# Optimization experiments

Measured on AMD Instinct MI355X. Metric: run time of the kernel, lower is better.

The kernel has to match this reference:

```python
import jax, jax.numpy as jnp
import numpy as np

_EPS = 1e-6


def setup_inputs() -> dict:
    key = jax.random.key(0)
    k1, k2, k3, k4 = jax.random.split(key, 4)
    B, N = 32, 131072
    xyz_s = jax.random.normal(k1, (B, 3, N), dtype=jnp.float32)
    weighted_t = jax.random.normal(k2, (B, 3, N), dtype=jnp.float32)
    weights = jax.random.uniform(k3, (B, 1, N), dtype=jnp.float32)
    label = jax.random.randint(k4, (B, 1, N), 0, 2).astype(jnp.float32)
    return {"xyz_s": xyz_s, "weighted_t": weighted_t, "weights": weights, "label": label}


def reference(xyz_s, weighted_t, weights, label):
    # background mask: |label - 1|
    background = jnp.abs(label - 1.0)            # (B,1,N)
    w = (weights * background)[:, 0, :]          # (B,N)
    xs = jnp.swapaxes(xyz_s, 1, 2)               # (B,N,3) source points
    xt = jnp.swapaxes(weighted_t, 1, 2)          # (B,N,3) target points

    # normalized weights
    wn = w[..., None] / (jnp.sum(w, axis=1, keepdims=True)[..., None] + _EPS)  # (B,N,1)

    # weighted centroids
    centroid_s = jnp.sum(xs * wn, axis=1)        # (B,3)
    centroid_t = jnp.sum(xt * wn, axis=1)        # (B,3)

    s_centered = xs - centroid_s[:, None, :]
    t_centered = xt - centroid_t[:, None, :]

    # weighted covariance: s_centered^T @ (t_centered * wn) -> (B,3,3)
    cov = jnp.einsum('bnd,bne->bde', s_centered, t_centered * wn)

    u, s, vh = jnp.linalg.svd(cov)               # cov = u @ diag(s) @ vh
    v = jnp.swapaxes(vh, -1, -2)
    ut = jnp.swapaxes(u, -1, -2)

    rot_pos = v @ ut
    v_neg = v.at[:, :, 2].multiply(-1.0)         # flip last column of V
    rot_neg = v_neg @ ut
    det_pos = jnp.linalg.det(rot_pos)
    rot = jnp.where(det_pos[:, None, None] > 0, rot_pos, rot_neg)  # (B,3,3)

    translation = -rot @ centroid_s[..., None] + centroid_t[..., None]  # (B,3,1)
    return rot, translation
```

## Files before the change

kernel.cpp:

```cpp
#include <hip/hip_runtime.h>
#include <math.h>

#define N_PTS 131072
#define BPB   64
#define CHUNK (N_PTS / BPB)
#define TPB   256
#define NACC  16
#define NITER (CHUNK / 4 / TPB)

__global__ __launch_bounds__(TPB) void ego_partial_kernel(
    const float* __restrict__ xyz_s,
    const float* __restrict__ wtgt,
    const float* __restrict__ weights,
    const float* __restrict__ label,
    float* __restrict__ partials)
{
    const int b     = blockIdx.y;
    const int chunk = blockIdx.x;
    const int t     = threadIdx.x;

    const size_t baseN  = (size_t)b * N_PTS + (size_t)chunk * CHUNK;
    const size_t base3  = (size_t)b * 3 * N_PTS + (size_t)chunk * CHUNK;

    const float4* w4  = (const float4*)(weights + baseN);
    const float4* l4  = (const float4*)(label   + baseN);
    const float4* xs0 = (const float4*)(xyz_s + base3);
    const float4* xs1 = (const float4*)(xyz_s + base3 + N_PTS);
    const float4* xs2 = (const float4*)(xyz_s + base3 + 2 * N_PTS);
    const float4* xt0 = (const float4*)(wtgt  + base3);
    const float4* xt1 = (const float4*)(wtgt  + base3 + N_PTS);
    const float4* xt2 = (const float4*)(wtgt  + base3 + 2 * N_PTS);

    float acc[NACC];
#pragma unroll
    for (int i = 0; i < NACC; ++i) acc[i] = 0.0f;

#pragma unroll
    for (int k = 0; k < NITER; ++k) {
        const int i = t + k * TPB;
        const float4 wv = w4[i];
        const float4 lv = l4[i];
        const float4 a0 = xs0[i], a1 = xs1[i], a2 = xs2[i];
        const float4 b0 = xt0[i], b1 = xt1[i], b2 = xt2[i];

#define ACCUM(C)                                              \
        {                                                     \
            const float w  = wv.C * fabsf(lv.C - 1.0f);       \
            const float s0 = a0.C, s1 = a1.C, s2 = a2.C;      \
            const float t0 = b0.C, t1 = b1.C, t2 = b2.C;      \
            acc[0] += w;                                      \
            const float ws0 = w * s0, ws1 = w * s1, ws2 = w * s2; \
            acc[1] += ws0;  acc[2] += ws1;  acc[3] += ws2;    \
            acc[4] += w * t0; acc[5] += w * t1; acc[6] += w * t2; \
            acc[7]  += ws0 * t0; acc[8]  += ws0 * t1; acc[9]  += ws0 * t2; \
            acc[10] += ws1 * t0; acc[11] += ws1 * t1; acc[12] += ws1 * t2; \
            acc[13] += ws2 * t0; acc[14] += ws2 * t1; acc[15] += ws2 * t2; \
        }
        ACCUM(x) ACCUM(y) ACCUM(z) ACCUM(w)
#undef ACCUM
    }

#pragma unroll
    for (int i = 0; i < NACC; ++i) {
        float v = acc[i];
#pragma unroll
        for (int off = 32; off > 0; off >>= 1)
            v += __shfl_down(v, off, 64);
        acc[i] = v;
    }

    __shared__ float red[TPB / 64][NACC];
    const int wave = t >> 6;
    const int lane = t & 63;
    if (lane == 0) {
#pragma unroll
        for (int i = 0; i < NACC; ++i) red[wave][i] = acc[i];
    }
    __syncthreads();

    if (t < NACC) {
        float v = 0.0f;
#pragma unroll
        for (int wv_ = 0; wv_ < TPB / 64; ++wv_) v += red[wv_][t];
        partials[((size_t)b * BPB + chunk) * NACC + t] = v;
    }
}

__global__ __launch_bounds__(64) void ego_finalize_kernel(
    const float* __restrict__ partials,
    float* __restrict__ out,
    int B)
{
    const int b = blockIdx.x;
    const int t = threadIdx.x;

    double acc[NACC];
    const float* p = partials + ((size_t)b * BPB + t) * NACC;
#pragma unroll
    for (int i = 0; i < NACC; ++i) acc[i] = (double)p[i];

#pragma unroll
    for (int i = 0; i < NACC; ++i) {
        double v = acc[i];
#pragma unroll
        for (int off = 32; off > 0; off >>= 1)
            v += __shfl_down(v, off, 64);
        acc[i] = v;
    }

    if (t != 0) return;

    const double W     = acc[0];
    const double denom = W + 1e-6;
    const double cs0 = acc[1] / denom, cs1 = acc[2] / denom, cs2 = acc[3] / denom;
    const double ct0 = acc[4] / denom, ct1 = acc[5] / denom, ct2 = acc[6] / denom;
    const double f   = 2.0 - W / denom;

    const double c00 = acc[7]  / denom - cs0 * ct0 * f;
    const double c01 = acc[8]  / denom - cs0 * ct1 * f;
    const double c02 = acc[9]  / denom - cs0 * ct2 * f;
    const double c10 = acc[10] / denom - cs1 * ct0 * f;
    const double c11 = acc[11] / denom - cs1 * ct1 * f;
    const double c12 = acc[12] / denom - cs1 * ct2 * f;
    const double c20 = acc[13] / denom - cs2 * ct0 * f;
    const double c21 = acc[14] / denom - cs2 * ct1 * f;
    const double c22 = acc[15] / denom - cs2 * ct2 * f;

    double b00 = c00*c00 + c10*c10 + c20*c20;
    double b01 = c00*c01 + c10*c11 + c20*c21;
    double b02 = c00*c02 + c10*c12 + c20*c22;
    double b11 = c01*c01 + c11*c11 + c21*c21;
    double b12 = c01*c02 + c11*c12 + c21*c22;
    double b22 = c02*c02 + c12*c12 + c22*c22;

    double v00 = 1, v01 = 0, v02 = 0;
    double v10 = 0, v11 = 1, v12 = 0;
    double v20 = 0, v21 = 0, v22 = 1;

#define JROT(bpp, bqq, bpq, bkp, bkq, vp0, vp1, vp2, vq0, vq1, vq2)   \
    if (fabs(bpq) > 1e-30) {                                          \
        const double tau = (bqq - bpp) / (2.0 * bpq);                 \
        const double jt  = (tau >= 0.0 ? 1.0 : -1.0) /                \
                           (fabs(tau) + sqrt(1.0 + tau * tau));       \
        const double jc  = 1.0 / sqrt(1.0 + jt * jt);                 \
        const double js  = jt * jc;                                   \
        bpp -= jt * bpq; bqq += jt * bpq; bpq = 0.0;                  \
        { const double kp = bkp, kq = bkq;                            \
          bkp = jc * kp - js * kq; bkq = js * kp + jc * kq; }         \
        { double x;                                                   \
          x = vp0; vp0 = jc * x - js * vq0; vq0 = js * x + jc * vq0;  \
          x = vp1; vp1 = jc * x - js * vq1; vq1 = js * x + jc * vq1;  \
          x = vp2; vp2 = jc * x - js * vq2; vq2 = js * x + jc * vq2; }\
    }

#pragma unroll
    for (int sweep = 0; sweep < 6; ++sweep) {
        JROT(b00, b11, b01, b02, b12, v00, v10, v20, v01, v11, v21)
        JROT(b00, b22, b02, b01, b12, v00, v10, v20, v02, v12, v22)
        JROT(b11, b22, b12, b01, b02, v01, v11, v21, v02, v12, v22)
    }
#undef JROT

    double l0 = b00, l1 = b11, l2 = b22;
#define CSWAP(la, lb, a0, a1, a2, q0, q1, q2)                         \
    if (lb > la) { double x;                                          \
        x = la; la = lb; lb = x;                                      \
        x = a0; a0 = q0; q0 = x;                                      \
        x = a1; a1 = q1; q1 = x;                                      \
        x = a2; a2 = q2; q2 = x; }
    CSWAP(l0, l1, v00, v10, v20, v01, v11, v21)
    CSWAP(l0, l2, v00, v10, v20, v02, v12, v22)
    CSWAP(l1, l2, v01, v11, v21, v02, v12, v22)
#undef CSWAP

#define MAKEU(vc0, vc1, vc2, u0, u1, u2)                              \
    double u0 = c00 * vc0 + c01 * vc1 + c02 * vc2;                    \
    double u1 = c10 * vc0 + c11 * vc1 + c12 * vc2;                    \
    double u2 = c20 * vc0 + c21 * vc1 + c22 * vc2;                    \
    { const double nn = sqrt(u0 * u0 + u1 * u1 + u2 * u2);            \
      const double r = (nn > 1e-150) ? 1.0 / nn : 0.0;                \
      u0 *= r; u1 *= r; u2 *= r; }
    MAKEU(v00, v10, v20, u00, u10, u20)
    MAKEU(v01, v11, v21, u01, u11, u21)
    MAKEU(v02, v12, v22, u02, u12, u22)
#undef MAKEU
    if (u02 * u02 + u12 * u12 + u22 * u22 < 0.5) {
        u02 = u10 * u21 - u20 * u11;
        u12 = u20 * u01 - u00 * u21;
        u22 = u00 * u11 - u10 * u01;
    }

    const double a00_ = v00*u00 + v01*u01, g00 = v02*u02;
    const double a01_ = v00*u10 + v01*u11, g01 = v02*u12;
    const double a02_ = v00*u20 + v01*u21, g02 = v02*u22;
    const double a10_ = v10*u00 + v11*u01, g10 = v12*u02;
    const double a11_ = v10*u10 + v11*u11, g11 = v12*u12;
    const double a12_ = v10*u20 + v11*u21, g12 = v12*u22;
    const double a20_ = v20*u00 + v21*u01, g20 = v22*u02;
    const double a21_ = v20*u10 + v21*u11, g21 = v22*u12;
    const double a22_ = v20*u20 + v21*u21, g22 = v22*u22;

    const double r00 = a00_ + g00, r01 = a01_ + g01, r02 = a02_ + g02;
    const double r10 = a10_ + g10, r11 = a11_ + g11, r12 = a12_ + g12;
    const double r20 = a20_ + g20, r21 = a21_ + g21, r22 = a22_ + g22;
    const double det = r00 * (r11 * r22 - r12 * r21)
                     - r01 * (r10 * r22 - r12 * r20)
                     + r02 * (r10 * r21 - r11 * r20);
    const double sgn = (det > 0.0) ? 1.0 : -1.0;

    const double R00 = a00_ + sgn * g00, R01 = a01_ + sgn * g01, R02 = a02_ + sgn * g02;
    const double R10 = a10_ + sgn * g10, R11 = a11_ + sgn * g11, R12 = a12_ + sgn * g12;
    const double R20 = a20_ + sgn * g20, R21 = a21_ + sgn * g21, R22 = a22_ + sgn * g22;

    const double t0 = -(R00 * cs0 + R01 * cs1 + R02 * cs2) + ct0;
    const double t1 = -(R10 * cs0 + R11 * cs1 + R12 * cs2) + ct1;
    const double t2 = -(R20 * cs0 + R21 * cs1 + R22 * cs2) + ct2;

    float* ro = out + (size_t)b * 9;
    ro[0] = (float)R00; ro[1] = (float)R01; ro[2] = (float)R02;
    ro[3] = (float)R10; ro[4] = (float)R11; ro[5] = (float)R12;
    ro[6] = (float)R20; ro[7] = (float)R21; ro[8] = (float)R22;
    float* to = out + (size_t)B * 9 + (size_t)b * 3;
    to[0] = (float)t0; to[1] = (float)t1; to[2] = (float)t2;
}

extern "C" void kernel_launch(void* const* d_in, const int* in_sizes, int n_in,
                              void* d_out, int out_size, void* d_ws, size_t ws_size,
                              hipStream_t stream) {
    const float* xyz_s   = (const float*)d_in[0];
    const float* wtgt    = (const float*)d_in[1];
    const float* weights = (const float*)d_in[2];
    const float* label   = (const float*)d_in[3];
    float* out = (float*)d_out;
    float* partials = (float*)d_ws;

    const int B = in_sizes[2] / N_PTS;

    dim3 grid1(BPB, B);
    ego_partial_kernel<<<grid1, TPB, 0, stream>>>(xyz_s, wtgt, weights, label, partials);
    ego_finalize_kernel<<<B, 64, 0, stream>>>(partials, out, B);
}
```

Before: 155.3 us.

## Stage chunk inputs into LDS via async global_load_lds before accumulation

Each wave now loads two of the eight input streams directly into shared memory with the global_load_lds builtin, and all threads then read the float4 data from LDS for the moment accumulation. The intent is to issue all global loads up front without spending VGPRs, and to get more memory requests in flight. This adds 64KB of LDS per block, which limits occupancy, plus an extra LDS round trip and a barrier. The reduction scratch now reuses the same LDS buffer. CHUNK is hardcoded to 2048, which still equals N_PTS/BPB.

```diff
diff --git a/kernel.cpp b/kernel.cpp
--- a/kernel.cpp
+++ b/kernel.cpp
@@ -3,10 +3,12 @@
 
 #define N_PTS 131072
 #define BPB   64
-#define CHUNK (N_PTS / BPB)
+#define CHUNK 2048
 #define TPB   256
 #define NACC  16
-#define NITER (CHUNK / 4 / TPB)
+
+typedef const __attribute__((address_space(1))) void gvoid_t;
+typedef __attribute__((address_space(3))) void lvoid_t;
 
 __global__ __launch_bounds__(TPB) void ego_partial_kernel(
     const float* __restrict__ xyz_s,
@@ -15,33 +17,62 @@
     const float* __restrict__ label,
     float* __restrict__ partials)
 {
-    const int b     = blockIdx.y;
-    const int chunk = blockIdx.x;
-    const int t     = threadIdx.x;
-
-    const size_t baseN  = (size_t)b * N_PTS + (size_t)chunk * CHUNK;
-    const size_t base3  = (size_t)b * 3 * N_PTS + (size_t)chunk * CHUNK;
-
-    const float4* w4  = (const float4*)(weights + baseN);
-    const float4* l4  = (const float4*)(label   + baseN);
-    const float4* xs0 = (const float4*)(xyz_s + base3);
-    const float4* xs1 = (const float4*)(xyz_s + base3 + N_PTS);
-    const float4* xs2 = (const float4*)(xyz_s + base3 + 2 * N_PTS);
-    const float4* xt0 = (const float4*)(wtgt  + base3);
-    const float4* xt1 = (const float4*)(wtgt  + base3 + N_PTS);
-    const float4* xt2 = (const float4*)(wtgt  + base3 + 2 * N_PTS);
+    __shared__ __align__(16) float lds[8][CHUNK];
+
+    const int b    = blockIdx.y;
+    const int c    = blockIdx.x;
+    const int t    = threadIdx.x;
+    const int wave = t >> 6;
+    const int lane = t & 63;
+
+    const size_t baseN = (size_t)b * N_PTS + (size_t)c * CHUNK;
+    const size_t base3 = (size_t)b * 3 * N_PTS + (size_t)c * CHUNK;
+
+    const float* g0;
+    const float* g1;
+    switch (wave) {
+        case 0:  g0 = weights + baseN;           g1 = label + baseN;            break;
+        case 1:  g0 = xyz_s + base3;             g1 = xyz_s + base3 + N_PTS;    break;
+        case 2:  g0 = xyz_s + base3 + 2*N_PTS;   g1 = wtgt  + base3;            break;
+        default: g0 = wtgt  + base3 + N_PTS;     g1 = wtgt  + base3 + 2*N_PTS;  break;
+    }
+    float* l0 = &lds[2 * wave][0];
+    float* l1 = &lds[2 * wave + 1][0];
+
+#pragma unroll
+    for (int j = 0; j < 8; ++j) {
+        const int off = j * 256 + lane * 4;
+        __builtin_amdgcn_global_load_lds((gvoid_t*)(g0 + off),
+                                         (lvoid_t*)(l0 + j * 256), 16, 0, 0);
+    }
+#pragma unroll
+    for (int j = 0; j < 8; ++j) {
+        const int off = j * 256 + lane * 4;
+        __builtin_amdgcn_global_load_lds((gvoid_t*)(g1 + off),
+                                         (lvoid_t*)(l1 + j * 256), 16, 0, 0);
+    }
+    __syncthreads();
+
+    const float4* W4 = (const float4*)lds[0];
+    const float4* L4 = (const float4*)lds[1];
+    const float4* A0 = (const float4*)lds[2];
+    const float4* A1 = (const float4*)lds[3];
+    const float4* A2 = (const float4*)lds[4];
+    const float4* B0 = (const float4*)lds[5];
+    const float4* B1 = (const float4*)lds[6];
+    const float4* B2 = (const float4*)lds[7];
 
     float acc[NACC];
 #pragma unroll
     for (int i = 0; i < NACC; ++i) acc[i] = 0.0f;
 
 #pragma unroll
-    for (int k = 0; k < NITER; ++k) {
+    for (int k = 0; k < CHUNK / 4 / TPB; ++k) {
         const int i = t + k * TPB;
-        const float4 wv = w4[i];
-        const float4 lv = l4[i];
-        const float4 a0 = xs0[i], a1 = xs1[i], a2 = xs2[i];
-        const float4 b0 = xt0[i], b1 = xt1[i], b2 = xt2[i];
+        const float4 wv = W4[i];
+        const float4 lv = L4[i];
+        const float4 a0 = A0[i], a1 = A1[i], a2 = A2[i];
+        const float4 b0 = B0[i], b1 = B1[i], b2 = B2[i];
 
 #define ACCUM(C)                                              \
         {                                                     \
@@ -69,20 +100,19 @@
         acc[i] = v;
     }
 
-    __shared__ float red[TPB / 64][NACC];
-    const int wave = t >> 6;
-    const int lane = t & 63;
+    __syncthreads();
+    float* red = (float*)lds;
     if (lane == 0) {
 #pragma unroll
-        for (int i = 0; i < NACC; ++i) red[wave][i] = acc[i];
+        for (int i = 0; i < NACC; ++i) red[wave * NACC + i] = acc[i];
     }
     __syncthreads();
 
     if (t < NACC) {
         float v = 0.0f;
 #pragma unroll
-        for (int wv_ = 0; wv_ < TPB / 64; ++wv_) v += red[wv_][t];
-        partials[((size_t)b * BPB + chunk) * NACC + t] = v;
+        for (int wv_ = 0; wv_ < TPB / 64; ++wv_) v += red[wv_ * NACC + t];
+        partials[((size_t)b * BPB + c) * NACC + t] = v;
     }
 }
 
```

Result: no change. 153.2 us (-1.4%).
